# Performance work log

Measured on AMD Instinct MI355X. Metric: run time of the kernel, lower is better.

## Reference

```python
import jax, jax.numpy as jnp
import numpy as np
from jax import lax

B, H, P_LEN, Q_LEN, T = 64, 512, 512, 64, 4
D = 2 * H  # 1024
NEG = -1e9


def setup_inputs() -> dict:
    key = jax.random.key(0)
    ks = jax.random.split(key, 12)
    sc = 0.02
    return {
        "H_p": jax.random.normal(ks[0], (B, D, P_LEN), jnp.float32),
        "H_q": jax.random.normal(ks[1], (B, D, Q_LEN), jnp.float32),
        "M": jax.random.normal(ks[2], (B, D, P_LEN), jnp.float32),
        "W_4": jax.random.normal(ks[3], (D, H), jnp.float32) * sc,
        "W_5": jax.random.normal(ks[4], (D, H), jnp.float32) * sc,
        "W_6": jax.random.normal(ks[5], (D, H), jnp.float32) * sc,
        "W_7": jax.random.normal(ks[6], (D, H), jnp.float32) * sc,
        "gru_W_ih": jax.random.normal(ks[7], (3 * D, D), jnp.float32) * sc,
        "gru_W_hh": jax.random.normal(ks[8], (3 * D, D), jnp.float32) * sc,
        "gru_b_ih": jnp.zeros((3 * D,), jnp.float32),
        "gru_b_hh": jnp.zeros((3 * D,), jnp.float32),
        "p_mask": jnp.ones((B, P_LEN), bool),
        "q_mask": jnp.ones((B, Q_LEN), bool),
    }


def _gru_cell(x, h, W_ih, W_hh, b_ih, b_hh):
    # PyTorch GRUCell math. x,h: [B, D]
    gi = x @ W_ih.T + b_ih
    gh = h @ W_hh.T + b_hh
    i_r, i_z, i_n = jnp.split(gi, 3, axis=-1)
    h_r, h_z, h_n = jnp.split(gh, 3, axis=-1)
    r = jax.nn.sigmoid(i_r + h_r)
    z = jax.nn.sigmoid(i_z + h_z)
    n = jnp.tanh(i_n + r * h_n)
    return (1.0 - z) * n + z * h


def reference(H_p, H_q, M, W_4, W_5, W_6, W_7, gru_W_ih, gru_W_hh, gru_b_ih, gru_b_hh, p_mask, q_mask):
    # Step-invariant projections (same math, hoisted out of the loop).
    proj_q = jnp.einsum('bdq,dh->bqh', H_q, W_4)  # [B,q,H]
    proj_p = jnp.einsum('bdp,dh->bph', M, W_6)    # [B,p,H]
    qm = jnp.where(q_mask, 0.0, NEG)              # [B,q]
    pm = jnp.where(p_mask, 0.0, NEG)              # [B,p]

    def step(h, _):
        # attention over question, conditioned on pointer state h
        sq = jnp.einsum('bqh,bh->bq', proj_q, h @ W_5) + qm
        alpha = jax.nn.softmax(sq, axis=-1)
        c = jnp.einsum('bdq,bq->bd', H_q, alpha)  # question context [B,D]
        # start-pointer distribution over passage (pre-update state)
        p1 = jax.nn.softmax(jnp.einsum('bph,bh->bp', proj_p, h @ W_7) + pm, axis=-1)
        # GRU state update fed by the attended context
        h_new = _gru_cell(c, h, gru_W_ih, gru_W_hh, gru_b_ih, gru_b_hh)
        # end-pointer distribution (post-update state)
        p2 = jax.nn.softmax(jnp.einsum('bph,bh->bp', proj_p, h_new @ W_7) + pm, axis=-1)
        return h_new, (p1, p2)

    h0 = jnp.zeros((H_p.shape[0], D), H_p.dtype)
    _, (p1s, p2s) = lax.scan(step, h0, None, length=T)
    return jnp.stack([p1s, p2s])  # [2, T, B, p_len]
```

## Files before the change

### kernel.cpp

```cpp
#include <hip/hip_runtime.h>
#include <math.h>

#define Bb   64
#define Dd   1024
#define Pp   512
#define Qq   64
#define Tt   4

typedef __attribute__((ext_vector_type(8))) short bf16x8;
typedef __attribute__((ext_vector_type(4))) float f32x4;
typedef unsigned short ushort_t;

__device__ __forceinline__ short f2bf(float f) {
    union { float f; unsigned u; } v; v.f = f;
    unsigned r = v.u + 0x7FFFu + ((v.u >> 16) & 1u);
    return (short)(r >> 16);
}
__device__ __forceinline__ float bf2f(short s) {
    union { unsigned u; float f; } v; v.u = ((unsigned)(unsigned short)s) << 16; return v.f;
}
__device__ __forceinline__ unsigned long long pack4bf(float a, float b, float c, float d) {
    return (unsigned long long)(unsigned short)f2bf(a)
         | ((unsigned long long)(unsigned short)f2bf(b) << 16)
         | ((unsigned long long)(unsigned short)f2bf(c) << 32)
         | ((unsigned long long)(unsigned short)f2bf(d) << 48);
}
__device__ __forceinline__ unsigned long long pack4s(short a, short b, short c, short d) {
    return (unsigned long long)(unsigned short)a
         | ((unsigned long long)(unsigned short)b << 16)
         | ((unsigned long long)(unsigned short)c << 32)
         | ((unsigned long long)(unsigned short)d << 48);
}

struct LoadA {
    const float* A; int lda;
    __device__ void operator()(short (*As)[72], int kg, int tid) const {
#pragma unroll
        for (int p = 0; p < 4; ++p) {
            const int i = tid + p * 256, r = i >> 4, c4 = (i & 15) * 4;
            const float4 v = *(const float4*)(A + (size_t)r * lda + kg + c4);
            *(unsigned long long*)&As[r][c4] = pack4bf(v.x, v.y, v.z, v.w);
        }
    }
};

template <bool BF16B, bool BF16OUT, class AF>
__device__ __forceinline__
void mf_core(short (*As)[72], short (*Bs)[72], const AF& af,
             const void* Bsrc, int ldb, void* Cv, int ldc,
             int kbeg, int ktiles)
{
    const int tid = threadIdx.x;
    const int w = tid >> 6, l = tid & 63;
    const int fr = l & 15, fk = (l >> 4) * 8;

    f32x4 acc[4][2] = {};

    for (int kt = 0; kt < ktiles; ++kt) {
        const int kg = kbeg + kt * 64;
        __syncthreads();
        af(As, kg, tid);
        if (BF16B) {
            const ushort_t* Bu = (const ushort_t*)Bsrc;
#pragma unroll
            for (int p = 0; p < 4; ++p) {
                const int i = tid + p * 256, r = i >> 3, c8 = (i & 7) * 8;
                *(float4*)&Bs[r][c8] = *(const float4*)(Bu + (size_t)r * ldb + kg + c8);
            }
        } else {
            const float* Bf = (const float*)Bsrc;
#pragma unroll
            for (int p = 0; p < 8; ++p) {
                const int i = tid + p * 256, r = i >> 4, c4 = (i & 15) * 4;
                const float4 v = *(const float4*)(Bf + (size_t)r * ldb + kg + c4);
                *(unsigned long long*)&Bs[r][c4] = pack4bf(v.x, v.y, v.z, v.w);
            }
        }
        __syncthreads();
#pragma unroll
        for (int h = 0; h < 2; ++h) {
            const int k0 = h * 32;
            bf16x8 a0 = *(const bf16x8*)&As[ 0 + fr][k0 + fk];
            bf16x8 a1 = *(const bf16x8*)&As[16 + fr][k0 + fk];
            bf16x8 a2 = *(const bf16x8*)&As[32 + fr][k0 + fk];
            bf16x8 a3 = *(const bf16x8*)&As[48 + fr][k0 + fk];
            bf16x8 b0 = *(const bf16x8*)&Bs[w * 32 + fr][k0 + fk];
            bf16x8 b1 = *(const bf16x8*)&Bs[w * 32 + 16 + fr][k0 + fk];
            acc[0][0] = __builtin_amdgcn_mfma_f32_16x16x32_bf16(a0, b0, acc[0][0], 0, 0, 0);
            acc[1][0] = __builtin_amdgcn_mfma_f32_16x16x32_bf16(a1, b0, acc[1][0], 0, 0, 0);
            acc[2][0] = __builtin_amdgcn_mfma_f32_16x16x32_bf16(a2, b0, acc[2][0], 0, 0, 0);
            acc[3][0] = __builtin_amdgcn_mfma_f32_16x16x32_bf16(a3, b0, acc[3][0], 0, 0, 0);
            acc[0][1] = __builtin_amdgcn_mfma_f32_16x16x32_bf16(a0, b1, acc[0][1], 0, 0, 0);
            acc[1][1] = __builtin_amdgcn_mfma_f32_16x16x32_bf16(a1, b1, acc[1][1], 0, 0, 0);
            acc[2][1] = __builtin_amdgcn_mfma_f32_16x16x32_bf16(a2, b1, acc[2][1], 0, 0, 0);
            acc[3][1] = __builtin_amdgcn_mfma_f32_16x16x32_bf16(a3, b1, acc[3][1], 0, 0, 0);
        }
    }
#pragma unroll
    for (int mi = 0; mi < 4; ++mi)
#pragma unroll
        for (int ni = 0; ni < 2; ++ni)
#pragma unroll
            for (int r = 0; r < 4; ++r) {
                const int row = mi * 16 + 4 * (l >> 4) + r;
                const int col = w * 32 + ni * 16 + fr;
                if (BF16OUT) ((ushort_t*)Cv)[(size_t)row * ldc + col] = (ushort_t)f2bf(acc[mi][ni][r]);
                else         ((float*)Cv)[(size_t)row * ldc + col] = acc[mi][ni][r];
            }
}

__device__ __forceinline__
void msplit_core(short* smbase, const float* A, int lda, const float* B, int ldb,
                 float* C, int ldc, int kbeg, int ktiles)
{
    short (*AsH)[72] = (short(*)[72])smbase;
    short (*AsL)[72] = (short(*)[72])(smbase + 4608);
    short (*BsH)[72] = (short(*)[72])(smbase + 9216);
    short (*BsL)[72] = (short(*)[72])(smbase + 18432);
    const int tid = threadIdx.x;
    const int w = tid >> 6, l = tid & 63;
    const int fr = l & 15, fk = (l >> 4) * 8;

    f32x4 acc[4][2] = {};

    for (int kt = 0; kt < ktiles; ++kt) {
        const int kg = kbeg + kt * 64;
        __syncthreads();
#pragma unroll
        for (int p = 0; p < 4; ++p) {
            const int i = tid + p * 256, r = i >> 4, c4 = (i & 15) * 4;
            const float4 v = *(const float4*)(A + (size_t)r * lda + kg + c4);
            const short h0 = f2bf(v.x), h1 = f2bf(v.y), h2 = f2bf(v.z), h3 = f2bf(v.w);
            *(unsigned long long*)&AsH[r][c4] = pack4s(h0, h1, h2, h3);
            *(unsigned long long*)&AsL[r][c4] = pack4bf(v.x - bf2f(h0), v.y - bf2f(h1),
                                                        v.z - bf2f(h2), v.w - bf2f(h3));
        }
#pragma unroll
        for (int p = 0; p < 8; ++p) {
            const int i = tid + p * 256, r = i >> 4, c4 = (i & 15) * 4;
            const float4 v = *(const float4*)(B + (size_t)r * ldb + kg + c4);
            const short h0 = f2bf(v.x), h1 = f2bf(v.y), h2 = f2bf(v.z), h3 = f2bf(v.w);
            *(unsigned long long*)&BsH[r][c4] = pack4s(h0, h1, h2, h3);
            *(unsigned long long*)&BsL[r][c4] = pack4bf(v.x - bf2f(h0), v.y - bf2f(h1),
                                                        v.z - bf2f(h2), v.w - bf2f(h3));
        }
        __syncthreads();
#pragma unroll
        for (int pass = 0; pass < 3; ++pass) {
            short (*Ap)[72] = (pass == 2) ? AsL : AsH;
            short (*Bp)[72] = (pass == 1) ? BsL : BsH;
#pragma unroll
            for (int h = 0; h < 2; ++h) {
                const int k0 = h * 32;
                bf16x8 a0 = *(const bf16x8*)&Ap[ 0 + fr][k0 + fk];
                bf16x8 a1 = *(const bf16x8*)&Ap[16 + fr][k0 + fk];
                bf16x8 a2 = *(const bf16x8*)&Ap[32 + fr][k0 + fk];
                bf16x8 a3 = *(const bf16x8*)&Ap[48 + fr][k0 + fk];
                bf16x8 b0 = *(const bf16x8*)&Bp[w * 32 + fr][k0 + fk];
                bf16x8 b1 = *(const bf16x8*)&Bp[w * 32 + 16 + fr][k0 + fk];
                acc[0][0] = __builtin_amdgcn_mfma_f32_16x16x32_bf16(a0, b0, acc[0][0], 0, 0, 0);
                acc[1][0] = __builtin_amdgcn_mfma_f32_16x16x32_bf16(a1, b0, acc[1][0], 0, 0, 0);
                acc[2][0] = __builtin_amdgcn_mfma_f32_16x16x32_bf16(a2, b0, acc[2][0], 0, 0, 0);
                acc[3][0] = __builtin_amdgcn_mfma_f32_16x16x32_bf16(a3, b0, acc[3][0], 0, 0, 0);
                acc[0][1] = __builtin_amdgcn_mfma_f32_16x16x32_bf16(a0, b1, acc[0][1], 0, 0, 0);
                acc[1][1] = __builtin_amdgcn_mfma_f32_16x16x32_bf16(a1, b1, acc[1][1], 0, 0, 0);
                acc[2][1] = __builtin_amdgcn_mfma_f32_16x16x32_bf16(a2, b1, acc[2][1], 0, 0, 0);
                acc[3][1] = __builtin_amdgcn_mfma_f32_16x16x32_bf16(a3, b1, acc[3][1], 0, 0, 0);
            }
        }
    }
#pragma unroll
    for (int mi = 0; mi < 4; ++mi)
#pragma unroll
        for (int ni = 0; ni < 2; ++ni)
#pragma unroll
            for (int r = 0; r < 4; ++r) {
                const int row = mi * 16 + 4 * (l >> 4) + r;
                const int col = w * 32 + ni * 16 + fr;
                C[(size_t)row * ldc + col] = acc[mi][ni][r];
            }
}

__global__ __launch_bounds__(256)
void k_prologue(const float* __restrict__ W4, const float* __restrict__ W5,
                const float* __restrict__ W6, const float* __restrict__ W7,
                const float* __restrict__ Whh, const float* __restrict__ Wih,
                const float* __restrict__ Hq,
                ushort_t* __restrict__ Wcat, ushort_t* __restrict__ WihB,
                float* __restrict__ W76T, float* __restrict__ c0)
{
    __shared__ __align__(16) short sm[27648];
    const int bid = blockIdx.x, tid = threadIdx.x;
    if (bid < 128) {
        short (*As)[72] = (short(*)[72])sm;
        short (*Bs)[72] = (short(*)[72])(sm + 4608);
        const int n0 = (bid & 7) * 128, m0 = (bid >> 3) * 64;
        LoadA af{W4 + (size_t)m0 * 512, 512};
        mf_core<false, true>(As, Bs, af, W5 + (size_t)n0 * 512, 512,
                             Wcat + (size_t)m0 * 1024 + n0, 1024, 0, 8);
    } else if (bid < 256) {
        const int sub = bid - 128;
        const int n0 = (sub & 7) * 128, m0 = (sub >> 3) * 64;
        msplit_core(sm, W6 + (size_t)m0 * 512, 512, W7 + (size_t)n0 * 512, 512,
                    W76T + (size_t)m0 * 1024 + n0, 1024, 0, 8);
    } else if (bid < 384) {
        const int sub = bid - 256;
        for (int i = sub * 256 + tid; i < 786432; i += 128 * 256) {
            const float4 a = ((const float4*)Whh)[i];
            *(unsigned long long*)(Wcat + 1048576 + (size_t)i * 4) = pack4bf(a.x, a.y, a.z, a.w);
            const float4 b = ((const float4*)Wih)[i];
            *(unsigned long long*)(WihB + (size_t)i * 4) = pack4bf(b.x, b.y, b.z, b.w);
        }
    } else {
        const int sub = bid - 384;
        for (int u = sub * 256 + tid; u < 65536; u += 32 * 256) {
            const float4* p = (const float4*)(Hq + (size_t)u * 64);
            float s = 0.f;
#pragma unroll
            for (int j = 0; j < 16; ++j) { const float4 v = p[j]; s += v.x + v.y + v.z + v.w; }
            c0[u] = s * (1.0f / 64.0f);
        }
    }
}

__global__ __launch_bounds__(256)
void k_S1(const float* __restrict__ h, const ushort_t* __restrict__ Wcat,
          float* __restrict__ uqp, float* __restrict__ ghp)
{
    __shared__ __align__(16) short sm[13824];
    short (*As)[72] = (short(*)[72])sm;
    short (*Bs)[72] = (short(*)[72])(sm + 4608);
    const int x = blockIdx.x, z = blockIdx.z;
    const int n0 = x * 128, kb = z * 128;
    LoadA af{h, 1024};
    float* C; int ldc;
    if (x < 8) { C = uqp + (size_t)z * 65536 + n0;               ldc = 1024; }
    else       { C = ghp + (size_t)z * 196608 + (n0 - 1024);     ldc = 3072; }
    mf_core<true, false>(As, Bs, af, Wcat + (size_t)n0 * 1024, 1024, C, ldc, kb, 2);
}

__global__ __launch_bounds__(256)
void k_S2(const float* __restrict__ cbf, const ushort_t* __restrict__ WihB,
          float* __restrict__ gip)
{
    __shared__ __align__(16) short sm[13824];
    short (*As)[72] = (short(*)[72])sm;
    short (*Bs)[72] = (short(*)[72])(sm + 4608);
    const int n0 = blockIdx.x * 128, z = blockIdx.z;
    LoadA af{cbf, 1024};
    mf_core<true, false>(As, Bs, af, WihB + (size_t)n0 * 1024, 1024,
                         gip + (size_t)z * 196608 + n0, 3072, z * 128, 2);
}

__global__ __launch_bounds__(256)
void k_UB(const float* __restrict__ Hs, const float* __restrict__ W76T,
          float* __restrict__ ubp)
{
    __shared__ __align__(16) short sm[27648];
    const int n0 = blockIdx.x * 128, m0 = blockIdx.y * 64, z = blockIdx.z;
    msplit_core(sm, Hs + (size_t)m0 * 1024, 1024, W76T + (size_t)n0 * 1024, 1024,
                ubp + (size_t)z * 262144 + (size_t)m0 * 1024 + n0, 1024,
                z * 256, 4);
}

__global__ __launch_bounds__(1024)
void attn_kernel(const float* __restrict__ uqp,
                 const float* __restrict__ Hq,
                 float* __restrict__ cbuf)
{
    __shared__ float uqs[Dd];
    __shared__ float part[16][Qq];
    __shared__ float alpha[Qq];

    const int b = blockIdx.x;
    const int tid = threadIdx.x;
    const float* hq = Hq + (size_t)b * Dd * Qq;
    const int q = tid & 63, g = tid >> 6;

    {
        const size_t o = (size_t)b * Dd + tid;
        float s = 0.f;
#pragma unroll
        for (int p = 0; p < 8; ++p) s += uqp[(size_t)p * 65536 + o];
        uqs[tid] = s;
    }
    __syncthreads();
    {
        float ps = 0.f;
        for (int d = g * 64; d < g * 64 + 64; ++d)
            ps += hq[(size_t)d * Qq + q] * uqs[d];
        part[g][q] = ps;
    }
    __syncthreads();
    if (tid < 64) {
        float sq = 0.f;
#pragma unroll
        for (int gg = 0; gg < 16; ++gg) sq += part[gg][tid];
        float mx = sq;
#pragma unroll
        for (int off = 32; off; off >>= 1) mx = fmaxf(mx, __shfl_xor(mx, off));
        const float e = expf(sq - mx);
        float sm = e;
#pragma unroll
        for (int off = 32; off; off >>= 1) sm += __shfl_xor(sm, off);
        alpha[tid] = e / sm;
    }
    __syncthreads();

    const float4* row = (const float4*)(hq + (size_t)tid * Qq);
    float cv = 0.f;
#pragma unroll
    for (int qq = 0; qq < 16; ++qq) {
        const float4 hv = row[qq];
        const float4 av = *(const float4*)&alpha[qq * 4];
        cv += hv.x * av.x + hv.y * av.y + hv.z * av.z + hv.w * av.w;
    }
    cbuf[(size_t)b * Dd + tid] = cv;
}

template <bool GH0>
__global__ __launch_bounds__(256)
void gru_elem(const float* __restrict__ gip, const float* __restrict__ ghp,
              const float* __restrict__ b_ih, const float* __restrict__ b_hh,
              const float* __restrict__ h_in, float* __restrict__ h_out)
{
    const int idx = blockIdx.x * 256 + threadIdx.x;
    const int d = idx & 1023;
    const size_t zs = (size_t)64 * 3072;
    const size_t base = (size_t)(idx >> 10) * 3072 + d;

    float ir = 0, iz = 0, in_ = 0, hr = 0, hz = 0, hn = 0;
#pragma unroll
    for (int z = 0; z < 8; ++z) {
        ir  += gip[z * zs + base];
        iz  += gip[z * zs + base + 1024];
        in_ += gip[z * zs + base + 2048];
    }
    if (!GH0) {
#pragma unroll
        for (int z = 0; z < 8; ++z) {
            hr += ghp[z * zs + base];
            hz += ghp[z * zs + base + 1024];
            hn += ghp[z * zs + base + 2048];
        }
    }
    ir += b_ih[d]; iz += b_ih[Dd + d]; in_ += b_ih[2 * Dd + d];
    hr += b_hh[d]; hz += b_hh[Dd + d]; hn += b_hh[2 * Dd + d];

    const float h = GH0 ? 0.f : h_in[idx];
    const float r = 1.f / (1.f + expf(-(ir + hr)));
    const float z = 1.f / (1.f + expf(-(iz + hz)));
    const float n = tanhf(in_ + r * hn);
    h_out[idx] = (1.f - z) * n + z * h;
}

__global__ __launch_bounds__(256)
void scores_kernel(const float* __restrict__ ubp,
                   const float* __restrict__ Mt,
                   float* __restrict__ sp)
{
    __shared__ float us[5][256];
    const int b = blockIdx.x;
    const int ds = blockIdx.y;
    const int tid = threadIdx.x;

    us[0][tid] = 0.f;
#pragma unroll
    for (int tt = 1; tt < 5; ++tt) {
        const size_t o = (size_t)((tt - 1) * 64 + b) * 1024 + ds * 256 + tid;
        us[tt][tid] = ubp[o] + ubp[o + 262144] + ubp[o + 2 * 262144] + ubp[o + 3 * 262144];
    }
    __syncthreads();

    float acc[5][2] = {};
    const float* mp = Mt + ((size_t)b * Dd + ds * 256) * Pp + tid;
    for (int dd = 0; dd < 256; ++dd) {
        float m0 = mp[0], m1 = mp[256];
#pragma unroll
        for (int tt = 0; tt < 5; ++tt) {
            float u = us[tt][dd];
            acc[tt][0] += u * m0;
            acc[tt][1] += u * m1;
        }
        mp += Pp;
    }
#pragma unroll
    for (int tt = 0; tt < 5; ++tt) {
        size_t o = ((size_t)(ds * Bb + b) * 5 + tt) * Pp + tid;
        sp[o] = acc[tt][0];
        sp[o + 256] = acc[tt][1];
    }
}

__global__ __launch_bounds__(256)
void final_softmax(const float* __restrict__ sp, float* __restrict__ out)
{
    __shared__ float red[8];
    const int bt = blockIdx.x;
    const int b = bt / 5, t = bt % 5;
    const int tid = threadIdx.x;

    float s0 = 0.f, s1 = 0.f;
#pragma unroll
    for (int ds = 0; ds < 4; ++ds) {
        size_t o = ((size_t)(ds * Bb + b) * 5 + t) * Pp + tid;
        s0 += sp[o];
        s1 += sp[o + 256];
    }

    float mx = fmaxf(s0, s1);
#pragma unroll
    for (int off = 32; off; off >>= 1) mx = fmaxf(mx, __shfl_xor(mx, off));
    if ((tid & 63) == 0) red[tid >> 6] = mx;
    __syncthreads();
    const float m = fmaxf(fmaxf(red[0], red[1]), fmaxf(red[2], red[3]));

    const float e0 = expf(s0 - m), e1 = expf(s1 - m);
    float sm = e0 + e1;
#pragma unroll
    for (int off = 32; off; off >>= 1) sm += __shfl_xor(sm, off);
    if ((tid & 63) == 0) red[4 + (tid >> 6)] = sm;
    __syncthreads();
    const float tot = red[4] + red[5] + red[6] + red[7];

    const float p0v = e0 / tot, p1v = e1 / tot;
    if (t < Tt) {
        size_t o = ((size_t)t * Bb + b) * Pp + tid;
        out[o] = p0v; out[o + 256] = p1v;
    }
    if (t >= 1) {
        size_t o = (size_t)Tt * Bb * Pp + ((size_t)(t - 1) * Bb + b) * Pp + tid;
        out[o] = p0v; out[o + 256] = p1v;
    }
}

extern "C" void kernel_launch(void* const* d_in, const int* in_sizes, int n_in,
                              void* d_out, int out_size, void* d_ws, size_t ws_size,
                              hipStream_t stream)
{
    const float* Hq  = (const float*)d_in[1];
    const float* Mt  = (const float*)d_in[2];
    const float* W4  = (const float*)d_in[3];
    const float* W5  = (const float*)d_in[4];
    const float* W6  = (const float*)d_in[5];
    const float* W7  = (const float*)d_in[6];
    const float* Wih = (const float*)d_in[7];
    const float* Whh = (const float*)d_in[8];
    const float* bih = (const float*)d_in[9];
    const float* bhh = (const float*)d_in[10];
    float* out = (float*)d_out;
    float* ws  = (float*)d_ws;
    (void)in_sizes; (void)n_in; (void)out_size; (void)ws_size;

    float* Hs   = ws;
    float* cbf  = ws + 262144;
    float* W76T = ws + 327680;
    float* uqp  = ws + 1376256;
    float* gip  = ws + 1900544;
    float* ghp  = ws + 3473408;
    float* spb  = ws + 5046272;
    ushort_t* Wcat = (ushort_t*)(ws + 5701632);
    ushort_t* WihB = (ushort_t*)(ws + 7798784);
    float* ubp  = gip;

    k_prologue<<<dim3(416), 256, 0, stream>>>(W4, W5, W6, W7, Whh, Wih, Hq,
                                              Wcat, WihB, W76T, cbf);

    k_S2<<<dim3(24, 1, 8), 256, 0, stream>>>(cbf, WihB, gip);
    gru_elem<true><<<dim3(256), 256, 0, stream>>>(gip, ghp, bih, bhh, Hs, Hs);

    for (int t = 1; t <= 3; ++t) {
        const float* h = Hs + (size_t)(t - 1) * 65536;
        k_S1<<<dim3(32, 1, 8), 256, 0, stream>>>(h, Wcat, uqp, ghp);
        attn_kernel<<<dim3(Bb), 1024, 0, stream>>>(uqp, Hq, cbf);
        k_S2<<<dim3(24, 1, 8), 256, 0, stream>>>(cbf, WihB, gip);
        gru_elem<false><<<dim3(256), 256, 0, stream>>>(gip, ghp, bih, bhh, h,
                                                       Hs + (size_t)t * 65536);
    }

    k_UB<<<dim3(8, 4, 4), 256, 0, stream>>>(Hs, W76T, ubp);
    scores_kernel<<<dim3(Bb, 4), 256, 0, stream>>>(ubp, Mt, spb);
    final_softmax<<<dim3(Bb * 5), 256, 0, stream>>>(spb, out);
}
```

Before: 186.0 us.

## Precompute per-batch question key matrix and fuse attention with Whh GEMM

Reassociates the question attention score: instead of forming W4·W5ᵀ and projecting h each step, it precomputes K[b,q,:] = (H_qᵀW4)W5ᵀ once per batch in bf16. Each step then scores by a direct dot of K with h. The attention softmax/context and the h·Whhᵀ GEMM are merged into one kernel launch, removing the uqp partial-sum round trip and one launch per step. The cost is a much larger prologue GEMM (64×64×512×1024) and per-step reads of an 8 MB bf16 K tensor.

```diff
diff --git a/kernel.cpp b/kernel.cpp
--- a/kernel.cpp
+++ b/kernel.cpp
@@ -43,8 +43,32 @@
         }
     }
 };
-
-template <bool BF16B, bool BF16OUT, class AF>
+struct LoadABf {
+    const ushort_t* A; int lda;
+    __device__ void operator()(short (*As)[72], int kg, int tid) const {
+#pragma unroll
+        for (int p = 0; p < 2; ++p) {
+            const int i = tid + p * 256, r = i >> 3, c8 = (i & 7) * 8;
+            *(float4*)&As[r][c8] = *(const float4*)(A + (size_t)r * lda + kg + c8);
+        }
+    }
+};
+struct LoadAT {
+    const float* Hqb;
+    __device__ void operator()(short (*As)[72], int kg, int tid) const {
+#pragma unroll
+        for (int p = 0; p < 4; ++p) {
+            const int i = tid + p * 256, r = i >> 4, c4 = (i & 15) * 4;
+            const float v0 = Hqb[(size_t)(kg + c4 + 0) * 64 + r];
+            const float v1 = Hqb[(size_t)(kg + c4 + 1) * 64 + r];
+            const float v2 = Hqb[(size_t)(kg + c4 + 2) * 64 + r];
+            const float v3 = Hqb[(size_t)(kg + c4 + 3) * 64 + r];
+            *(unsigned long long*)&As[r][c4] = pack4bf(v0, v1, v2, v3);
+        }
+    }
+};
+
+template <int BMODE, bool BF16OUT, class AF>
 __device__ __forceinline__
 void mf_core(short (*As)[72], short (*Bs)[72], const AF& af,
              const void* Bsrc, int ldb, void* Cv, int ldc,
@@ -60,20 +84,30 @@
         const int kg = kbeg + kt * 64;
         __syncthreads();
         af(As, kg, tid);
-        if (BF16B) {
+        if (BMODE == 1) {
             const ushort_t* Bu = (const ushort_t*)Bsrc;
 #pragma unroll
             for (int p = 0; p < 4; ++p) {
                 const int i = tid + p * 256, r = i >> 3, c8 = (i & 7) * 8;
                 *(float4*)&Bs[r][c8] = *(const float4*)(Bu + (size_t)r * ldb + kg + c8);
             }
-        } else {
+        } else if (BMODE == 0) {
             const float* Bf = (const float*)Bsrc;
 #pragma unroll
             for (int p = 0; p < 8; ++p) {
                 const int i = tid + p * 256, r = i >> 4, c4 = (i & 15) * 4;
                 const float4 v = *(const float4*)(Bf + (size_t)r * ldb + kg + c4);
                 *(unsigned long long*)&Bs[r][c4] = pack4bf(v.x, v.y, v.z, v.w);
+            }
+        } else {
+            const float* Bf = (const float*)Bsrc;
+#pragma unroll
+            for (int p = 0; p < 8; ++p) {
+                const int i = tid + p * 256;
+                const int kk = i >> 5, n4 = (i & 31) * 4;
+                const float4 v = *(const float4*)(Bf + (size_t)(kg + kk) * ldb + n4);
+                Bs[n4 + 0][kk] = f2bf(v.x); Bs[n4 + 1][kk] = f2bf(v.y);
+                Bs[n4 + 2][kk] = f2bf(v.z); Bs[n4 + 3][kk] = f2bf(v.w);
             }
         }
         __syncthreads();
@@ -182,37 +216,37 @@
 }
 
 __global__ __launch_bounds__(256)
-void k_prologue(const float* __restrict__ W4, const float* __restrict__ W5,
-                const float* __restrict__ W6, const float* __restrict__ W7,
-                const float* __restrict__ Whh, const float* __restrict__ Wih,
-                const float* __restrict__ Hq,
-                ushort_t* __restrict__ Wcat, ushort_t* __restrict__ WihB,
-                float* __restrict__ W76T, float* __restrict__ c0)
+void k_P1(const float* __restrict__ W4, const float* __restrict__ W6,
+          const float* __restrict__ W7, const float* __restrict__ Whh,
+          const float* __restrict__ Wih, const float* __restrict__ Hq,
+          ushort_t* __restrict__ PQb, float* __restrict__ W76T,
+          ushort_t* __restrict__ WhhB, ushort_t* __restrict__ WihB,
+          float* __restrict__ c0)
 {
     __shared__ __align__(16) short sm[27648];
     const int bid = blockIdx.x, tid = threadIdx.x;
     if (bid < 128) {
-        short (*As)[72] = (short(*)[72])sm;
-        short (*Bs)[72] = (short(*)[72])(sm + 4608);
         const int n0 = (bid & 7) * 128, m0 = (bid >> 3) * 64;
-        LoadA af{W4 + (size_t)m0 * 512, 512};
-        mf_core<false, true>(As, Bs, af, W5 + (size_t)n0 * 512, 512,
-                             Wcat + (size_t)m0 * 1024 + n0, 1024, 0, 8);
-    } else if (bid < 256) {
-        const int sub = bid - 128;
-        const int n0 = (sub & 7) * 128, m0 = (sub >> 3) * 64;
         msplit_core(sm, W6 + (size_t)m0 * 512, 512, W7 + (size_t)n0 * 512, 512,
                     W76T + (size_t)m0 * 1024 + n0, 1024, 0, 8);
     } else if (bid < 384) {
-        const int sub = bid - 256;
+        const int sub = bid - 128;
+        const int b = sub >> 2, n0 = (sub & 3) * 128;
+        short (*As)[72] = (short(*)[72])sm;
+        short (*Bs)[72] = (short(*)[72])(sm + 4608);
+        LoadAT af{Hq + (size_t)b * 65536};
+        mf_core<2, true>(As, Bs, af, W4 + n0, 512,
+                         PQb + (size_t)b * 64 * 512 + n0, 512, 0, 16);
+    } else if (bid < 512) {
+        const int sub = bid - 384;
         for (int i = sub * 256 + tid; i < 786432; i += 128 * 256) {
             const float4 a = ((const float4*)Whh)[i];
-            *(unsigned long long*)(Wcat + 1048576 + (size_t)i * 4) = pack4bf(a.x, a.y, a.z, a.w);
-            const float4 b = ((const float4*)Wih)[i];
-            *(unsigned long long*)(WihB + (size_t)i * 4) = pack4bf(b.x, b.y, b.z, b.w);
+            *(unsigned long long*)(WhhB + (size_t)i * 4) = pack4bf(a.x, a.y, a.z, a.w);
+            const float4 c = ((const float4*)Wih)[i];
+            *(unsigned long long*)(WihB + (size_t)i * 4) = pack4bf(c.x, c.y, c.z, c.w);
         }
     } else {
-        const int sub = bid - 384;
+        const int sub = bid - 512;
         for (int u = sub * 256 + tid; u < 65536; u += 32 * 256) {
             const float4* p = (const float4*)(Hq + (size_t)u * 64);
             float s = 0.f;
@@ -224,19 +258,97 @@
 }
 
 __global__ __launch_bounds__(256)
-void k_S1(const float* __restrict__ h, const ushort_t* __restrict__ Wcat,
-          float* __restrict__ uqp, float* __restrict__ ghp)
+void k_P2(const ushort_t* __restrict__ PQb, const float* __restrict__ W5,
+          const float* __restrict__ c0, const ushort_t* __restrict__ WihB,
+          ushort_t* __restrict__ Kb, float* __restrict__ gip)
 {
     __shared__ __align__(16) short sm[13824];
     short (*As)[72] = (short(*)[72])sm;
     short (*Bs)[72] = (short(*)[72])(sm + 4608);
-    const int x = blockIdx.x, z = blockIdx.z;
-    const int n0 = x * 128, kb = z * 128;
-    LoadA af{h, 1024};
-    float* C; int ldc;
-    if (x < 8) { C = uqp + (size_t)z * 65536 + n0;               ldc = 1024; }
-    else       { C = ghp + (size_t)z * 196608 + (n0 - 1024);     ldc = 3072; }
-    mf_core<true, false>(As, Bs, af, Wcat + (size_t)n0 * 1024, 1024, C, ldc, kb, 2);
+    const int bid = blockIdx.x;
+    if (bid < 512) {
+        const int mt = bid >> 3, n0 = (bid & 7) * 128;
+        LoadABf af{PQb + (size_t)mt * 64 * 512, 512};
+        mf_core<0, true>(As, Bs, af, W5 + (size_t)n0 * 512, 512,
+                         Kb + (size_t)mt * 64 * 1024 + n0, 1024, 0, 8);
+    } else {
+        const int sub = bid - 512;
+        const int n0 = (sub >> 3) * 128, z = sub & 7;
+        LoadA af{c0, 1024};
+        mf_core<1, false>(As, Bs, af, WihB + (size_t)n0 * 1024, 1024,
+                          gip + (size_t)z * 196608 + n0, 3072, z * 128, 2);
+    }
+}
+
+__global__ __launch_bounds__(256)
+void k_mega1(const float* __restrict__ h, const ushort_t* __restrict__ Kb,
+             const float* __restrict__ Hq, const ushort_t* __restrict__ WhhB,
+             float* __restrict__ cbuf, float* __restrict__ ghp)
+{
+    __shared__ __align__(16) short sm[13824];
+    const int bid = blockIdx.x, tid = threadIdx.x;
+    if (bid < 256) {
+        float* smf = (float*)sm;
+        float* hs    = smf;
+        float* part  = smf + 1056;
+        float* alpha = smf + 1312;
+        const int b = bid >> 2, quarter = bid & 3;
+        {
+            const int d = tid * 4, g = tid >> 6;
+            const float4 v = *(const float4*)(h + (size_t)b * 1024 + d);
+            *(float4*)&hs[g * 264 + (d & 255)] = v;
+        }
+        __syncthreads();
+        {
+            const int q = tid >> 2, g = tid & 3;
+            const ushort_t* kr = Kb + ((size_t)(b * 64 + q) * 1024) + g * 256;
+            const float* hp = &hs[g * 264];
+            float s = 0.f;
+#pragma unroll
+            for (int kk = 0; kk < 256; kk += 8) {
+                const float4 pk = *(const float4*)(kr + kk);
+                const ushort_t* pu = (const ushort_t*)&pk;
+#pragma unroll
+                for (int j = 0; j < 8; ++j)
+                    s += bf2f((short)pu[j]) * hp[kk + j];
+            }
+            part[q * 4 + g] = s;
+        }
+        __syncthreads();
+        if (tid < 64) {
+            const float4 pv = *(const float4*)&part[tid * 4];
+            float sq = pv.x + pv.y + pv.z + pv.w;
+            float mx = sq;
+#pragma unroll
+            for (int off = 32; off; off >>= 1) mx = fmaxf(mx, __shfl_xor(mx, off));
+            const float e = expf(sq - mx);
+            float se = e;
+#pragma unroll
+            for (int off = 32; off; off >>= 1) se += __shfl_xor(se, off);
+            alpha[tid] = e / se;
+        }
+        __syncthreads();
+        {
+            const int d = quarter * 256 + tid;
+            const float4* row = (const float4*)(Hq + (size_t)b * 65536 + (size_t)d * 64);
+            float cv = 0.f;
+#pragma unroll
+            for (int qq = 0; qq < 16; ++qq) {
+                const float4 hv = row[qq];
+                const float4 av = *(const float4*)&alpha[qq * 4];
+                cv += hv.x * av.x + hv.y * av.y + hv.z * av.z + hv.w * av.w;
+            }
+            cbuf[(size_t)b * 1024 + d] = cv;
+        }
+    } else {
+        const int sub = bid - 256;
+        const int n0 = (sub >> 3) * 128, z = sub & 7;
+        short (*As)[72] = (short(*)[72])sm;
+        short (*Bs)[72] = (short(*)[72])(sm + 4608);
+        LoadA af{h, 1024};
+        mf_core<1, false>(As, Bs, af, WhhB + (size_t)n0 * 1024, 1024,
+                          ghp + (size_t)z * 196608 + n0, 3072, z * 128, 2);
+    }
 }
 
 __global__ __launch_bounds__(256)
@@ -246,10 +358,10 @@
     __shared__ __align__(16) short sm[13824];
     short (*As)[72] = (short(*)[72])sm;
     short (*Bs)[72] = (short(*)[72])(sm + 4608);
-    const int n0 = blockIdx.x * 128, z = blockIdx.z;
+    const int n0 = (blockIdx.x >> 3) * 128, z = blockIdx.x & 7;
     LoadA af{cbf, 1024};
-    mf_core<true, false>(As, Bs, af, WihB + (size_t)n0 * 1024, 1024,
-                         gip + (size_t)z * 196608 + n0, 3072, z * 128, 2);
+    mf_core<1, false>(As, Bs, af, WihB + (size_t)n0 * 1024, 1024,
+                      gip + (size_t)z * 196608 + n0, 3072, z * 128, 2);
 }
 
 __global__ __launch_bounds__(256)
@@ -261,61 +373,6 @@
     msplit_core(sm, Hs + (size_t)m0 * 1024, 1024, W76T + (size_t)n0 * 1024, 1024,
                 ubp + (size_t)z * 262144 + (size_t)m0 * 1024 + n0, 1024,
                 z * 256, 4);
-}
-
-__global__ __launch_bounds__(1024)
-void attn_kernel(const float* __restrict__ uqp,
-                 const float* __restrict__ Hq,
-                 float* __restrict__ cbuf)
-{
-    __shared__ float uqs[Dd];
-    __shared__ float part[16][Qq];
-    __shared__ float alpha[Qq];
-
-    const int b = blockIdx.x;
-    const int tid = threadIdx.x;
-    const float* hq = Hq + (size_t)b * Dd * Qq;
-    const int q = tid & 63, g = tid >> 6;
-
-    {
-        const size_t o = (size_t)b * Dd + tid;
-        float s = 0.f;
-#pragma unroll
-        for (int p = 0; p < 8; ++p) s += uqp[(size_t)p * 65536 + o];
-        uqs[tid] = s;
-    }
-    __syncthreads();
-    {
-        float ps = 0.f;
-        for (int d = g * 64; d < g * 64 + 64; ++d)
-            ps += hq[(size_t)d * Qq + q] * uqs[d];
-        part[g][q] = ps;
-    }
-    __syncthreads();
-    if (tid < 64) {
-        float sq = 0.f;
-#pragma unroll
-        for (int gg = 0; gg < 16; ++gg) sq += part[gg][tid];
-        float mx = sq;
-#pragma unroll
-        for (int off = 32; off; off >>= 1) mx = fmaxf(mx, __shfl_xor(mx, off));
-        const float e = expf(sq - mx);
-        float sm = e;
-#pragma unroll
-        for (int off = 32; off; off >>= 1) sm += __shfl_xor(sm, off);
-        alpha[tid] = e / sm;
-    }
-    __syncthreads();
-
-    const float4* row = (const float4*)(hq + (size_t)tid * Qq);
-    float cv = 0.f;
-#pragma unroll
-    for (int qq = 0; qq < 16; ++qq) {
-        const float4 hv = row[qq];
-        const float4 av = *(const float4*)&alpha[qq * 4];
-        cv += hv.x * av.x + hv.y * av.y + hv.z * av.z + hv.w * av.w;
-    }
-    cbuf[(size_t)b * Dd + tid] = cv;
 }
 
 template <bool GH0>
@@ -455,25 +512,25 @@
     float* Hs   = ws;
     float* cbf  = ws + 262144;
     float* W76T = ws + 327680;
-    float* uqp  = ws + 1376256;
-    float* gip  = ws + 1900544;
-    float* ghp  = ws + 3473408;
-    float* spb  = ws + 5046272;
-    ushort_t* Wcat = (ushort_t*)(ws + 5701632);
-    ushort_t* WihB = (ushort_t*)(ws + 7798784);
+    float* gip  = ws + 1376256;
+    float* ghp  = ws + 2949120;
+    float* spb  = ws + 4521984;
+    ushort_t* Kb   = (ushort_t*)(ws + 5177344);
+    ushort_t* WhhB = (ushort_t*)(ws + 7274496);
+    ushort_t* WihB = (ushort_t*)(ws + 8847360);
+    ushort_t* PQb  = (ushort_t*)ghp;
     float* ubp  = gip;
 
-    k_prologue<<<dim3(416), 256, 0, stream>>>(W4, W5, W6, W7, Whh, Wih, Hq,
-                                              Wcat, WihB, W76T, cbf);
-
-    k_S2<<<dim3(24, 1, 8), 256, 0, stream>>>(cbf, WihB, gip);
+    k_P1<<<dim3(544), 256, 0, stream>>>(W4, W6, W7, Whh, Wih, Hq,
+                                        PQb, W76T, WhhB, WihB, cbf);
+    k_P2<<<dim3(704), 256, 0, stream>>>(PQb, W5, cbf, WihB, Kb, gip);
+
     gru_elem<true><<<dim3(256), 256, 0, stream>>>(gip, ghp, bih, bhh, Hs, Hs);
 
     for (int t = 1; t <= 3; ++t) {
         const float* h = Hs + (size_t)(t - 1) * 65536;
-        k_S1<<<dim3(32, 1, 8), 256, 0, stream>>>(h, Wcat, uqp, ghp);
-        attn_kernel<<<dim3(Bb), 1024, 0, stream>>>(uqp, Hq, cbf);
-        k_S2<<<dim3(24, 1, 8), 256, 0, stream>>>(cbf, WihB, gip);
+        k_mega1<<<dim3(448), 256, 0, stream>>>(h, Kb, Hq, WhhB, cbf, ghp);
+        k_S2<<<dim3(192), 256, 0, stream>>>(cbf, WihB, gip);
         gru_elem<false><<<dim3(256), 256, 0, stream>>>(gip, ghp, bih, bhh, h,
                                                        Hs + (size_t)t * 65536);
     }
```

New measurement: 233.5 us. +25.6%, slower.

## Fuse attention into GRU hidden GEMM kernel, computing h·W54 per batch inline

Applied to the files above, without the earlier changes.

Merges the per-step k_S1 GEMM and attn_kernel into one launch. 64 blocks each compute the query projection h·(W5 W4^T) for one batch row with a scalar dot-product loop over a bf16 weight, then do softmax and the context reduction. The other 192 blocks compute the W_hh GEMM partials. This removes one launch per step and the uqp partial-sum round trip through memory. In exchange, each attention block now streams the full 2 MB bf16 W54T matrix with scalar FMAs instead of MFMA, which could make those blocks the critical path.

```diff
diff --git a/kernel.cpp b/kernel.cpp
--- a/kernel.cpp
+++ b/kernel.cpp
@@ -44,7 +44,7 @@
     }
 };
 
-template <bool BF16B, bool BF16OUT, class AF>
+template <int BMODE, bool BF16OUT, class AF>
 __device__ __forceinline__
 void mf_core(short (*As)[72], short (*Bs)[72], const AF& af,
              const void* Bsrc, int ldb, void* Cv, int ldc,
@@ -60,7 +60,7 @@
         const int kg = kbeg + kt * 64;
         __syncthreads();
         af(As, kg, tid);
-        if (BF16B) {
+        if (BMODE == 1) {
             const ushort_t* Bu = (const ushort_t*)Bsrc;
 #pragma unroll
             for (int p = 0; p < 4; ++p) {
@@ -182,34 +182,35 @@
 }
 
 __global__ __launch_bounds__(256)
-void k_prologue(const float* __restrict__ W4, const float* __restrict__ W5,
-                const float* __restrict__ W6, const float* __restrict__ W7,
-                const float* __restrict__ Whh, const float* __restrict__ Wih,
-                const float* __restrict__ Hq,
-                ushort_t* __restrict__ Wcat, ushort_t* __restrict__ WihB,
-                float* __restrict__ W76T, float* __restrict__ c0)
+void k_P1(const float* __restrict__ W4, const float* __restrict__ W5,
+          const float* __restrict__ W6, const float* __restrict__ W7,
+          const float* __restrict__ Whh, const float* __restrict__ Wih,
+          const float* __restrict__ Hq,
+          ushort_t* __restrict__ W54T, float* __restrict__ W76T,
+          ushort_t* __restrict__ WhhB, ushort_t* __restrict__ WihB,
+          float* __restrict__ c0)
 {
     __shared__ __align__(16) short sm[27648];
     const int bid = blockIdx.x, tid = threadIdx.x;
     if (bid < 128) {
-        short (*As)[72] = (short(*)[72])sm;
-        short (*Bs)[72] = (short(*)[72])(sm + 4608);
         const int n0 = (bid & 7) * 128, m0 = (bid >> 3) * 64;
-        LoadA af{W4 + (size_t)m0 * 512, 512};
-        mf_core<false, true>(As, Bs, af, W5 + (size_t)n0 * 512, 512,
-                             Wcat + (size_t)m0 * 1024 + n0, 1024, 0, 8);
+        msplit_core(sm, W6 + (size_t)m0 * 512, 512, W7 + (size_t)n0 * 512, 512,
+                    W76T + (size_t)m0 * 1024 + n0, 1024, 0, 8);
     } else if (bid < 256) {
         const int sub = bid - 128;
         const int n0 = (sub & 7) * 128, m0 = (sub >> 3) * 64;
-        msplit_core(sm, W6 + (size_t)m0 * 512, 512, W7 + (size_t)n0 * 512, 512,
-                    W76T + (size_t)m0 * 1024 + n0, 1024, 0, 8);
+        short (*As)[72] = (short(*)[72])sm;
+        short (*Bs)[72] = (short(*)[72])(sm + 4608);
+        LoadA af{W4 + (size_t)m0 * 512, 512};
+        mf_core<0, true>(As, Bs, af, W5 + (size_t)n0 * 512, 512,
+                         W54T + (size_t)m0 * 1024 + n0, 1024, 0, 8);
     } else if (bid < 384) {
         const int sub = bid - 256;
         for (int i = sub * 256 + tid; i < 786432; i += 128 * 256) {
             const float4 a = ((const float4*)Whh)[i];
-            *(unsigned long long*)(Wcat + 1048576 + (size_t)i * 4) = pack4bf(a.x, a.y, a.z, a.w);
-            const float4 b = ((const float4*)Wih)[i];
-            *(unsigned long long*)(WihB + (size_t)i * 4) = pack4bf(b.x, b.y, b.z, b.w);
+            *(unsigned long long*)(WhhB + (size_t)i * 4) = pack4bf(a.x, a.y, a.z, a.w);
+            const float4 c = ((const float4*)Wih)[i];
+            *(unsigned long long*)(WihB + (size_t)i * 4) = pack4bf(c.x, c.y, c.z, c.w);
         }
     } else {
         const int sub = bid - 384;
@@ -224,32 +225,101 @@
 }
 
 __global__ __launch_bounds__(256)
-void k_S1(const float* __restrict__ h, const ushort_t* __restrict__ Wcat,
-          float* __restrict__ uqp, float* __restrict__ ghp)
+void k_mega(const float* __restrict__ h, const ushort_t* __restrict__ W54T,
+            const float* __restrict__ Hq, const ushort_t* __restrict__ WhhB,
+            float* __restrict__ cbuf, float* __restrict__ ghp)
+{
+    __shared__ __align__(16) short sm[13824];
+    const int bid = blockIdx.x, tid = threadIdx.x;
+    if (bid < 64) {
+        float* smf   = (float*)sm;
+        float* hs    = smf;
+        float* uqs   = smf + 1024;
+        float* part  = smf + 2048;
+        float* alpha = smf + 2304;
+        const int b = bid;
+        const float* hq = Hq + (size_t)b * 65536;
+
+        {
+#pragma unroll
+            for (int jj = 0; jj < 4; ++jj)
+                hs[jj * 256 + tid] = h[(size_t)b * 1024 + jj * 256 + tid];
+        }
+        __syncthreads();
+        {
+#pragma unroll
+            for (int jj = 0; jj < 4; ++jj) {
+                const int d = jj * 256 + tid;
+                const ushort_t* wr = W54T + (size_t)d * 1024;
+                float u = 0.f;
+                for (int kk = 0; kk < 1024; kk += 8) {
+                    const float4 pk = *(const float4*)(wr + kk);
+                    const ushort_t* pu = (const ushort_t*)&pk;
+#pragma unroll
+                    for (int j = 0; j < 8; ++j)
+                        u += bf2f((short)pu[j]) * hs[kk + j];
+                }
+                uqs[d] = u;
+            }
+        }
+        __syncthreads();
+        {
+            const int q = tid & 63, g = tid >> 6;
+            float s = 0.f;
+            for (int d = g * 256; d < g * 256 + 256; ++d)
+                s += hq[(size_t)d * 64 + q] * uqs[d];
+            part[g * 64 + q] = s;
+        }
+        __syncthreads();
+        if (tid < 64) {
+            float sq = part[tid] + part[64 + tid] + part[128 + tid] + part[192 + tid];
+            float mx = sq;
+#pragma unroll
+            for (int off = 32; off; off >>= 1) mx = fmaxf(mx, __shfl_xor(mx, off));
+            const float e = expf(sq - mx);
+            float se = e;
+#pragma unroll
+            for (int off = 32; off; off >>= 1) se += __shfl_xor(se, off);
+            alpha[tid] = e / se;
+        }
+        __syncthreads();
+        {
+#pragma unroll
+            for (int jj = 0; jj < 4; ++jj) {
+                const int d = jj * 256 + tid;
+                const float4* row = (const float4*)(hq + (size_t)d * 64);
+                float cv = 0.f;
+#pragma unroll
+                for (int qq = 0; qq < 16; ++qq) {
+                    const float4 hv = row[qq];
+                    const float4 av = *(const float4*)&alpha[qq * 4];
+                    cv += hv.x * av.x + hv.y * av.y + hv.z * av.z + hv.w * av.w;
+                }
+                cbuf[(size_t)b * 1024 + d] = cv;
+            }
+        }
+    } else {
+        const int sub = bid - 64;
+        const int n0 = (sub >> 3) * 128, z = sub & 7;
+        short (*As)[72] = (short(*)[72])sm;
+        short (*Bs)[72] = (short(*)[72])(sm + 4608);
+        LoadA af{h, 1024};
+        mf_core<1, false>(As, Bs, af, WhhB + (size_t)n0 * 1024, 1024,
+                          ghp + (size_t)z * 196608 + n0, 3072, z * 128, 2);
+    }
+}
+
+__global__ __launch_bounds__(256)
+void k_S2(const float* __restrict__ cbf, const ushort_t* __restrict__ WihB,
+          float* __restrict__ gip)
 {
     __shared__ __align__(16) short sm[13824];
     short (*As)[72] = (short(*)[72])sm;
     short (*Bs)[72] = (short(*)[72])(sm + 4608);
-    const int x = blockIdx.x, z = blockIdx.z;
-    const int n0 = x * 128, kb = z * 128;
-    LoadA af{h, 1024};
-    float* C; int ldc;
-    if (x < 8) { C = uqp + (size_t)z * 65536 + n0;               ldc = 1024; }
-    else       { C = ghp + (size_t)z * 196608 + (n0 - 1024);     ldc = 3072; }
-    mf_core<true, false>(As, Bs, af, Wcat + (size_t)n0 * 1024, 1024, C, ldc, kb, 2);
-}
-
-__global__ __launch_bounds__(256)
-void k_S2(const float* __restrict__ cbf, const ushort_t* __restrict__ WihB,
-          float* __restrict__ gip)
-{
-    __shared__ __align__(16) short sm[13824];
-    short (*As)[72] = (short(*)[72])sm;
-    short (*Bs)[72] = (short(*)[72])(sm + 4608);
-    const int n0 = blockIdx.x * 128, z = blockIdx.z;
+    const int n0 = (blockIdx.x >> 3) * 128, z = blockIdx.x & 7;
     LoadA af{cbf, 1024};
-    mf_core<true, false>(As, Bs, af, WihB + (size_t)n0 * 1024, 1024,
-                         gip + (size_t)z * 196608 + n0, 3072, z * 128, 2);
+    mf_core<1, false>(As, Bs, af, WihB + (size_t)n0 * 1024, 1024,
+                      gip + (size_t)z * 196608 + n0, 3072, z * 128, 2);
 }
 
 __global__ __launch_bounds__(256)
@@ -261,61 +331,6 @@
     msplit_core(sm, Hs + (size_t)m0 * 1024, 1024, W76T + (size_t)n0 * 1024, 1024,
                 ubp + (size_t)z * 262144 + (size_t)m0 * 1024 + n0, 1024,
                 z * 256, 4);
-}
-
-__global__ __launch_bounds__(1024)
-void attn_kernel(const float* __restrict__ uqp,
-                 const float* __restrict__ Hq,
-                 float* __restrict__ cbuf)
-{
-    __shared__ float uqs[Dd];
-    __shared__ float part[16][Qq];
-    __shared__ float alpha[Qq];
-
-    const int b = blockIdx.x;
-    const int tid = threadIdx.x;
-    const float* hq = Hq + (size_t)b * Dd * Qq;
-    const int q = tid & 63, g = tid >> 6;
-
-    {
-        const size_t o = (size_t)b * Dd + tid;
-        float s = 0.f;
-#pragma unroll
-        for (int p = 0; p < 8; ++p) s += uqp[(size_t)p * 65536 + o];
-        uqs[tid] = s;
-    }
-    __syncthreads();
-    {
-        float ps = 0.f;
-        for (int d = g * 64; d < g * 64 + 64; ++d)
-            ps += hq[(size_t)d * Qq + q] * uqs[d];
-        part[g][q] = ps;
-    }
-    __syncthreads();
-    if (tid < 64) {
-        float sq = 0.f;
-#pragma unroll
-        for (int gg = 0; gg < 16; ++gg) sq += part[gg][tid];
-        float mx = sq;
-#pragma unroll
-        for (int off = 32; off; off >>= 1) mx = fmaxf(mx, __shfl_xor(mx, off));
-        const float e = expf(sq - mx);
-        float sm = e;
-#pragma unroll
-        for (int off = 32; off; off >>= 1) sm += __shfl_xor(sm, off);
-        alpha[tid] = e / sm;
-    }
-    __syncthreads();
-
-    const float4* row = (const float4*)(hq + (size_t)tid * Qq);
-    float cv = 0.f;
-#pragma unroll
-    for (int qq = 0; qq < 16; ++qq) {
-        const float4 hv = row[qq];
-        const float4 av = *(const float4*)&alpha[qq * 4];
-        cv += hv.x * av.x + hv.y * av.y + hv.z * av.z + hv.w * av.w;
-    }
-    cbuf[(size_t)b * Dd + tid] = cv;
 }
 
 template <bool GH0>
@@ -455,25 +470,24 @@
     float* Hs   = ws;
     float* cbf  = ws + 262144;
     float* W76T = ws + 327680;
-    float* uqp  = ws + 1376256;
-    float* gip  = ws + 1900544;
-    float* ghp  = ws + 3473408;
-    float* spb  = ws + 5046272;
-    ushort_t* Wcat = (ushort_t*)(ws + 5701632);
-    ushort_t* WihB = (ushort_t*)(ws + 7798784);
+    float* gip  = ws + 1376256;
+    float* ghp  = ws + 2949120;
+    float* spb  = ws + 4521984;
+    ushort_t* W54T = (ushort_t*)(ws + 5177344);
+    ushort_t* WhhB = (ushort_t*)(ws + 5701632);
+    ushort_t* WihB = (ushort_t*)(ws + 7274496);
     float* ubp  = gip;
 
-    k_prologue<<<dim3(416), 256, 0, stream>>>(W4, W5, W6, W7, Whh, Wih, Hq,
-                                              Wcat, WihB, W76T, cbf);
-
-    k_S2<<<dim3(24, 1, 8), 256, 0, stream>>>(cbf, WihB, gip);
+    k_P1<<<dim3(416), 256, 0, stream>>>(W4, W5, W6, W7, Whh, Wih, Hq,
+                                        W54T, W76T, WhhB, WihB, cbf);
+
+    k_S2<<<dim3(192), 256, 0, stream>>>(cbf, WihB, gip);
     gru_elem<true><<<dim3(256), 256, 0, stream>>>(gip, ghp, bih, bhh, Hs, Hs);
 
     for (int t = 1; t <= 3; ++t) {
         const float* h = Hs + (size_t)(t - 1) * 65536;
-        k_S1<<<dim3(32, 1, 8), 256, 0, stream>>>(h, Wcat, uqp, ghp);
-        attn_kernel<<<dim3(Bb), 1024, 0, stream>>>(uqp, Hq, cbf);
-        k_S2<<<dim3(24, 1, 8), 256, 0, stream>>>(cbf, WihB, gip);
+        k_mega<<<dim3(256), 256, 0, stream>>>(h, W54T, Hq, WhhB, cbf, ghp);
+        k_S2<<<dim3(192), 256, 0, stream>>>(cbf, WihB, gip);
         gru_elem<false><<<dim3(256), 256, 0, stream>>>(gip, ghp, bih, bhh, h,
                                                        Hs + (size_t)t * 65536);
     }
```

After: 511.3 us. 175% more time.

## Fold per-step W76 projection into step kernel and use bf16 Hq in attention

Applied to the files above, without the earlier changes.

The final batched h·W76 projection over all hidden states is split up, and each step's share is computed inside the per-step GEMM kernel as extra blocks, so it runs alongside the gate GEMMs. Only the last state's projection stays as a small kernel at the end. Hq is converted to bf16 once in the prologue and the attention kernel reads it at half the bytes. Grids are flattened to 1D and the workspace layout is reorganised. This trades a bigger per-step launch and bf16 rounding of Hq for less serial tail work and less memory traffic.

```diff
diff --git a/kernel.cpp b/kernel.cpp
--- a/kernel.cpp
+++ b/kernel.cpp
@@ -44,7 +44,7 @@
     }
 };
 
-template <bool BF16B, bool BF16OUT, class AF>
+template <int BMODE, bool BF16OUT, class AF>
 __device__ __forceinline__
 void mf_core(short (*As)[72], short (*Bs)[72], const AF& af,
              const void* Bsrc, int ldb, void* Cv, int ldc,
@@ -60,7 +60,7 @@
         const int kg = kbeg + kt * 64;
         __syncthreads();
         af(As, kg, tid);
-        if (BF16B) {
+        if (BMODE == 1) {
             const ushort_t* Bu = (const ushort_t*)Bsrc;
 #pragma unroll
             for (int p = 0; p < 4; ++p) {
@@ -182,37 +182,44 @@
 }
 
 __global__ __launch_bounds__(256)
-void k_prologue(const float* __restrict__ W4, const float* __restrict__ W5,
-                const float* __restrict__ W6, const float* __restrict__ W7,
-                const float* __restrict__ Whh, const float* __restrict__ Wih,
-                const float* __restrict__ Hq,
-                ushort_t* __restrict__ Wcat, ushort_t* __restrict__ WihB,
-                float* __restrict__ W76T, float* __restrict__ c0)
+void k_P1(const float* __restrict__ W4, const float* __restrict__ W5,
+          const float* __restrict__ W6, const float* __restrict__ W7,
+          const float* __restrict__ Whh, const float* __restrict__ Wih,
+          const float* __restrict__ Hq,
+          ushort_t* __restrict__ W54T, float* __restrict__ W76T,
+          ushort_t* __restrict__ WhhB, ushort_t* __restrict__ WihB,
+          ushort_t* __restrict__ HqB, float* __restrict__ c0)
 {
     __shared__ __align__(16) short sm[27648];
     const int bid = blockIdx.x, tid = threadIdx.x;
     if (bid < 128) {
-        short (*As)[72] = (short(*)[72])sm;
-        short (*Bs)[72] = (short(*)[72])(sm + 4608);
         const int n0 = (bid & 7) * 128, m0 = (bid >> 3) * 64;
-        LoadA af{W4 + (size_t)m0 * 512, 512};
-        mf_core<false, true>(As, Bs, af, W5 + (size_t)n0 * 512, 512,
-                             Wcat + (size_t)m0 * 1024 + n0, 1024, 0, 8);
+        msplit_core(sm, W6 + (size_t)m0 * 512, 512, W7 + (size_t)n0 * 512, 512,
+                    W76T + (size_t)m0 * 1024 + n0, 1024, 0, 8);
     } else if (bid < 256) {
         const int sub = bid - 128;
         const int n0 = (sub & 7) * 128, m0 = (sub >> 3) * 64;
-        msplit_core(sm, W6 + (size_t)m0 * 512, 512, W7 + (size_t)n0 * 512, 512,
-                    W76T + (size_t)m0 * 1024 + n0, 1024, 0, 8);
+        short (*As)[72] = (short(*)[72])sm;
+        short (*Bs)[72] = (short(*)[72])(sm + 4608);
+        LoadA af{W4 + (size_t)m0 * 512, 512};
+        mf_core<0, true>(As, Bs, af, W5 + (size_t)n0 * 512, 512,
+                         W54T + (size_t)m0 * 1024 + n0, 1024, 0, 8);
     } else if (bid < 384) {
         const int sub = bid - 256;
         for (int i = sub * 256 + tid; i < 786432; i += 128 * 256) {
             const float4 a = ((const float4*)Whh)[i];
-            *(unsigned long long*)(Wcat + 1048576 + (size_t)i * 4) = pack4bf(a.x, a.y, a.z, a.w);
-            const float4 b = ((const float4*)Wih)[i];
-            *(unsigned long long*)(WihB + (size_t)i * 4) = pack4bf(b.x, b.y, b.z, b.w);
+            *(unsigned long long*)(WhhB + (size_t)i * 4) = pack4bf(a.x, a.y, a.z, a.w);
+            const float4 c = ((const float4*)Wih)[i];
+            *(unsigned long long*)(WihB + (size_t)i * 4) = pack4bf(c.x, c.y, c.z, c.w);
+        }
+    } else if (bid < 448) {
+        const int sub = bid - 384;
+        for (int i = sub * 256 + tid; i < 1048576; i += 64 * 256) {
+            const float4 a = ((const float4*)Hq)[i];
+            *(unsigned long long*)(HqB + (size_t)i * 4) = pack4bf(a.x, a.y, a.z, a.w);
         }
     } else {
-        const int sub = bid - 384;
+        const int sub = bid - 448;
         for (int u = sub * 256 + tid; u < 65536; u += 32 * 256) {
             const float4* p = (const float4*)(Hq + (size_t)u * 64);
             float s = 0.f;
@@ -224,48 +231,59 @@
 }
 
 __global__ __launch_bounds__(256)
-void k_S1(const float* __restrict__ h, const ushort_t* __restrict__ Wcat,
-          float* __restrict__ uqp, float* __restrict__ ghp)
+void k_SA(const float* __restrict__ h, const ushort_t* __restrict__ W54T,
+          const ushort_t* __restrict__ WhhB, const float* __restrict__ W76T,
+          float* __restrict__ uqp, float* __restrict__ ghp,
+          float* __restrict__ ubt)
+{
+    __shared__ __align__(16) short sm[27648];
+    const int bid = blockIdx.x;
+    if (bid < 256) {
+        short (*As)[72] = (short(*)[72])sm;
+        short (*Bs)[72] = (short(*)[72])(sm + 4608);
+        const int x = bid >> 3, z = bid & 7;
+        const int n0 = x * 128, kb = z * 128;
+        LoadA af{h, 1024};
+        if (x < 8)
+            mf_core<1, false>(As, Bs, af, W54T + (size_t)n0 * 1024, 1024,
+                              uqp + (size_t)z * 65536 + n0, 1024, kb, 2);
+        else
+            mf_core<1, false>(As, Bs, af, WhhB + (size_t)(n0 - 1024) * 1024, 1024,
+                              ghp + (size_t)z * 196608 + (n0 - 1024), 3072, kb, 2);
+    } else {
+        const int sub = bid - 256;
+        const int n0 = (sub & 7) * 128, z = sub >> 3;
+        msplit_core(sm, h, 1024, W76T + (size_t)n0 * 1024, 1024,
+                    ubt + (size_t)z * 262144 + n0, 1024, z * 256, 4);
+    }
+}
+
+__global__ __launch_bounds__(256)
+void k_S2(const float* __restrict__ cbf, const ushort_t* __restrict__ WihB,
+          float* __restrict__ gip)
 {
     __shared__ __align__(16) short sm[13824];
     short (*As)[72] = (short(*)[72])sm;
     short (*Bs)[72] = (short(*)[72])(sm + 4608);
-    const int x = blockIdx.x, z = blockIdx.z;
-    const int n0 = x * 128, kb = z * 128;
-    LoadA af{h, 1024};
-    float* C; int ldc;
-    if (x < 8) { C = uqp + (size_t)z * 65536 + n0;               ldc = 1024; }
-    else       { C = ghp + (size_t)z * 196608 + (n0 - 1024);     ldc = 3072; }
-    mf_core<true, false>(As, Bs, af, Wcat + (size_t)n0 * 1024, 1024, C, ldc, kb, 2);
-}
-
-__global__ __launch_bounds__(256)
-void k_S2(const float* __restrict__ cbf, const ushort_t* __restrict__ WihB,
-          float* __restrict__ gip)
-{
-    __shared__ __align__(16) short sm[13824];
-    short (*As)[72] = (short(*)[72])sm;
-    short (*Bs)[72] = (short(*)[72])(sm + 4608);
-    const int n0 = blockIdx.x * 128, z = blockIdx.z;
+    const int n0 = (blockIdx.x >> 3) * 128, z = blockIdx.x & 7;
     LoadA af{cbf, 1024};
-    mf_core<true, false>(As, Bs, af, WihB + (size_t)n0 * 1024, 1024,
-                         gip + (size_t)z * 196608 + n0, 3072, z * 128, 2);
-}
-
-__global__ __launch_bounds__(256)
-void k_UB(const float* __restrict__ Hs, const float* __restrict__ W76T,
-          float* __restrict__ ubp)
+    mf_core<1, false>(As, Bs, af, WihB + (size_t)n0 * 1024, 1024,
+                      gip + (size_t)z * 196608 + n0, 3072, z * 128, 2);
+}
+
+__global__ __launch_bounds__(256)
+void k_UB4(const float* __restrict__ h4, const float* __restrict__ W76T,
+           float* __restrict__ ubt)
 {
     __shared__ __align__(16) short sm[27648];
-    const int n0 = blockIdx.x * 128, m0 = blockIdx.y * 64, z = blockIdx.z;
-    msplit_core(sm, Hs + (size_t)m0 * 1024, 1024, W76T + (size_t)n0 * 1024, 1024,
-                ubp + (size_t)z * 262144 + (size_t)m0 * 1024 + n0, 1024,
-                z * 256, 4);
+    const int n0 = (blockIdx.x & 7) * 128, z = blockIdx.x >> 3;
+    msplit_core(sm, h4, 1024, W76T + (size_t)n0 * 1024, 1024,
+                ubt + (size_t)z * 262144 + n0, 1024, z * 256, 4);
 }
 
 __global__ __launch_bounds__(1024)
 void attn_kernel(const float* __restrict__ uqp,
-                 const float* __restrict__ Hq,
+                 const ushort_t* __restrict__ HqB,
                  float* __restrict__ cbuf)
 {
     __shared__ float uqs[Dd];
@@ -274,7 +292,7 @@
 
     const int b = blockIdx.x;
     const int tid = threadIdx.x;
-    const float* hq = Hq + (size_t)b * Dd * Qq;
+    const ushort_t* hq = HqB + (size_t)b * 65536;
     const int q = tid & 63, g = tid >> 6;
 
     {
@@ -288,7 +306,7 @@
     {
         float ps = 0.f;
         for (int d = g * 64; d < g * 64 + 64; ++d)
-            ps += hq[(size_t)d * Qq + q] * uqs[d];
+            ps += bf2f((short)hq[(size_t)d * 64 + q]) * uqs[d];
         part[g][q] = ps;
     }
     __syncthreads();
@@ -300,22 +318,25 @@
 #pragma unroll
         for (int off = 32; off; off >>= 1) mx = fmaxf(mx, __shfl_xor(mx, off));
         const float e = expf(sq - mx);
-        float sm = e;
-#pragma unroll
-        for (int off = 32; off; off >>= 1) sm += __shfl_xor(sm, off);
-        alpha[tid] = e / sm;
+        float se = e;
+#pragma unroll
+        for (int off = 32; off; off >>= 1) se += __shfl_xor(se, off);
+        alpha[tid] = e / se;
     }
     __syncthreads();
-
-    const float4* row = (const float4*)(hq + (size_t)tid * Qq);
-    float cv = 0.f;
-#pragma unroll
-    for (int qq = 0; qq < 16; ++qq) {
-        const float4 hv = row[qq];
-        const float4 av = *(const float4*)&alpha[qq * 4];
-        cv += hv.x * av.x + hv.y * av.y + hv.z * av.z + hv.w * av.w;
-    }
-    cbuf[(size_t)b * Dd + tid] = cv;
+    {
+        const float4* row = (const float4*)(hq + (size_t)tid * 64);
+        float cv = 0.f;
+#pragma unroll
+        for (int qq = 0; qq < 8; ++qq) {
+            const float4 pk = row[qq];
+            const ushort_t* pu = (const ushort_t*)&pk;
+#pragma unroll
+            for (int j = 0; j < 8; ++j)
+                cv += bf2f((short)pu[j]) * alpha[qq * 8 + j];
+        }
+        cbuf[(size_t)b * Dd + tid] = cv;
+    }
 }
 
 template <bool GH0>
@@ -458,27 +479,30 @@
     float* uqp  = ws + 1376256;
     float* gip  = ws + 1900544;
     float* ghp  = ws + 3473408;
-    float* spb  = ws + 5046272;
-    ushort_t* Wcat = (ushort_t*)(ws + 5701632);
-    ushort_t* WihB = (ushort_t*)(ws + 7798784);
-    float* ubp  = gip;
-
-    k_prologue<<<dim3(416), 256, 0, stream>>>(W4, W5, W6, W7, Whh, Wih, Hq,
-                                              Wcat, WihB, W76T, cbf);
-
-    k_S2<<<dim3(24, 1, 8), 256, 0, stream>>>(cbf, WihB, gip);
+    float* ubp  = ws + 5046272;
+    ushort_t* W54T = (ushort_t*)(ws + 6094848);
+    ushort_t* WhhB = (ushort_t*)(ws + 6619136);
+    ushort_t* WihB = (ushort_t*)(ws + 8192000);
+    ushort_t* HqB  = (ushort_t*)(ws + 9764864);
+    float* spb  = gip;
+
+    k_P1<<<dim3(480), 256, 0, stream>>>(W4, W5, W6, W7, Whh, Wih, Hq,
+                                        W54T, W76T, WhhB, WihB, HqB, cbf);
+
+    k_S2<<<dim3(192), 256, 0, stream>>>(cbf, WihB, gip);
     gru_elem<true><<<dim3(256), 256, 0, stream>>>(gip, ghp, bih, bhh, Hs, Hs);
 
     for (int t = 1; t <= 3; ++t) {
         const float* h = Hs + (size_t)(t - 1) * 65536;
-        k_S1<<<dim3(32, 1, 8), 256, 0, stream>>>(h, Wcat, uqp, ghp);
-        attn_kernel<<<dim3(Bb), 1024, 0, stream>>>(uqp, Hq, cbf);
-        k_S2<<<dim3(24, 1, 8), 256, 0, stream>>>(cbf, WihB, gip);
+        k_SA<<<dim3(288), 256, 0, stream>>>(h, W54T, WhhB, W76T, uqp, ghp,
+                                            ubp + (size_t)(t - 1) * 65536);
+        attn_kernel<<<dim3(Bb), 1024, 0, stream>>>(uqp, HqB, cbf);
+        k_S2<<<dim3(192), 256, 0, stream>>>(cbf, WihB, gip);
         gru_elem<false><<<dim3(256), 256, 0, stream>>>(gip, ghp, bih, bhh, h,
                                                        Hs + (size_t)t * 65536);
     }
 
-    k_UB<<<dim3(8, 4, 4), 256, 0, stream>>>(Hs, W76T, ubp);
+    k_UB4<<<dim3(32), 256, 0, stream>>>(Hs + 3 * 65536, W76T, ubp + 3 * 65536);
     scores_kernel<<<dim3(Bb, 4), 256, 0, stream>>>(ubp, Mt, spb);
     final_softmax<<<dim3(Bb * 5), 256, 0, stream>>>(spb, out);
 }
```

Result: faster. 180.2 us, median of 3 (-3.1%).
